# Kernel optimization log

Measured on AMD Instinct MI355X. Metric: run time of the kernel, lower is better.

The kernel has to match this reference:

```python
import jax, jax.numpy as jnp
import numpy as np

N_QUBITS = 12
N_LAYERS = 6
BATCH = 256
INPUT_DIM = 256
OUT_DIM = 64
PI = float(np.pi)


def _ry_mat(a):
    # a: scalar or (B,) real angle -> (...,2,2) complex64 RY matrix
    c, s = jnp.cos(a * 0.5), jnp.sin(a * 0.5)
    return jnp.stack([jnp.stack([c, -s], -1), jnp.stack([s, c], -1)], -2).astype(jnp.complex64)


def _rz_mat(a):
    # diag(e^{-i a/2}, e^{+i a/2})
    em = jnp.exp(-0.5j * a.astype(jnp.complex64))
    ep = jnp.exp(0.5j * a.astype(jnp.complex64))
    z = jnp.zeros_like(em)
    return jnp.stack([jnp.stack([em, z], -1), jnp.stack([z, ep], -1)], -2)


def _apply_1q(state, U, w):
    # shared (2,2) gate on wire w; state: (B, 2, ..., 2)
    s = jnp.moveaxis(state, w + 1, -1)
    s = jnp.einsum('ij,b...j->b...i', U, s)
    return jnp.moveaxis(s, -1, w + 1)


def _apply_1q_batched(state, U, w):
    # per-sample (B,2,2) gate on wire w
    s = jnp.moveaxis(state, w + 1, -1)
    s = jnp.einsum('bij,b...j->b...i', U, s)
    return jnp.moveaxis(s, -1, w + 1)


def _cnot(state, c, t):
    s0 = jnp.take(state, 0, axis=c + 1)
    s1 = jnp.take(state, 1, axis=c + 1)
    t_ax = t + 1 if t < c else t  # target axis index after removing control axis
    s1 = jnp.flip(s1, axis=t_ax)
    return jnp.stack([s0, s1], axis=c + 1)


def _cz(state, c, t):
    idx = [slice(None)] * (N_QUBITS + 1)
    idx[c + 1] = 1
    idx[t + 1] = 1
    return state.at[tuple(idx)].multiply(-1.0)


def _run_circuit(xq, q_weights):
    # xq: (B, n_qubits) in [-1,1]; forward passes xq*pi, circuit multiplies by pi again
    B = xq.shape[0]
    enc = xq * (PI * PI)
    state = jnp.zeros((B, 2 ** N_QUBITS), jnp.complex64).at[:, 0].set(1.0)
    state = state.reshape((B,) + (2,) * N_QUBITS)
    for i in range(N_QUBITS):
        state = _apply_1q_batched(state, _ry_mat(enc[:, i]), i)
    w = q_weights.reshape(N_LAYERS, N_QUBITS, 3)
    for layer in range(N_LAYERS):
        for i in range(N_QUBITS):
            # PennyLane order: RZ(w0) then RY(w1) then RZ(w2) -> U = RZ2 @ RY1 @ RZ0
            U = _rz_mat(w[layer, i, 2]) @ _ry_mat(w[layer, i, 1]) @ _rz_mat(w[layer, i, 0])
            state = _apply_1q(state, U, i)
        for i in range(N_QUBITS):
            state = _cnot(state, i, (i + 1) % N_QUBITS)
        if layer % 2 == 0 and layer < N_LAYERS - 1:
            for i in range(N_QUBITS):
                state = _apply_1q_batched(state, _ry_mat(enc[:, i] * 0.5), i)
        if layer % 2 == 1:
            for i in range(0, N_QUBITS - 2, 2):
                state = _cz(state, i, i + 2)
    # PauliZ expectation on wires 0,1,2
    p = (state.real ** 2 + state.imag ** 2).reshape(B, 2, 2, 2, -1).sum(-1)  # (B,2,2,2)
    z0 = (p[:, 0] - p[:, 1]).sum((-1, -2))
    z1 = (p[:, :, 0] - p[:, :, 1]).sum((-1, -2))
    z2 = (p[:, :, :, 0] - p[:, :, :, 1]).sum((-1, -2))
    return jnp.stack([z0, z1, z2], -1)  # (B, 3) float32


def _layernorm(h, g, b, eps=1e-5):
    mu = h.mean(-1, keepdims=True)
    var = ((h - mu) ** 2).mean(-1, keepdims=True)
    return (h - mu) * jax.lax.rsqrt(var + eps) * g + b


def _forward(x, W1, b1, g_ln, b_ln, W2, b2, W3, b3, q_weights, W4, b4, W5, b5):
    gelu = lambda t: jax.nn.gelu(t, approximate=False)
    h = gelu(x @ W1.T + b1)
    h = _layernorm(h, g_ln, b_ln)
    h = gelu(h @ W2.T + b2)
    xq = jnp.tanh(h @ W3.T + b3)  # (B, n_qubits)
    q = _run_circuit(xq, q_weights)  # (B, 3)
    return gelu(q @ W4.T + b4) @ W5.T + b5  # (B, OUT_DIM)


def setup_inputs() -> dict:
    key = jax.random.key(0)
    ks = jax.random.split(key, 8)
    rn = lambda k, shape, s=0.05: (jax.random.normal(k, shape) * s).astype(jnp.float32)
    return {
        'x': jax.random.normal(ks[0], (BATCH, INPUT_DIM), jnp.float32),
        'W1': rn(ks[1], (128, INPUT_DIM)), 'b1': jnp.zeros(128, jnp.float32),
        'g_ln': jnp.ones(128, jnp.float32), 'b_ln': jnp.zeros(128, jnp.float32),
        'W2': rn(ks[2], (64, 128)), 'b2': jnp.zeros(64, jnp.float32),
        'W3': rn(ks[3], (N_QUBITS, 64)), 'b3': jnp.zeros(N_QUBITS, jnp.float32),
        'q_weights': (jax.random.normal(ks[4], (N_LAYERS * N_QUBITS * 3,)) * 0.1).astype(jnp.float32),
        'W4': rn(ks[5], (32, 3)), 'b4': jnp.zeros(32, jnp.float32),
        'W5': rn(ks[6], (OUT_DIM, 32)), 'b5': jnp.zeros(OUT_DIM, jnp.float32),
    }


def reference(x, W1, b1, g_ln, b_ln, W2, b2, W3, b3, q_weights, W4, b4, W5, b5):
    return _forward(x, W1, b1, g_ln, b_ln, W2, b2, W3, b3, q_weights, W4, b4, W5, b5)
```

## Files before the change

### kernel.cpp

```cpp
#include <hip/hip_runtime.h>
#include <math.h>

#define NQ   12
#define NL   6
#define DIM  4096
#define BATCH 256
#define PI2  9.869604401089358f

__device__ __forceinline__ float geluf(float x) {
    return 0.5f * x * (1.0f + erff(x * 0.70710678118654752f));
}

__device__ __forceinline__ int slotf(int j) { return j + (j >> 4); }

__device__ __forceinline__ float2 cmul(float2 a, float2 b) {
    return make_float2(fmaf(a.x, b.x, -a.y * b.y), fmaf(a.x, b.y, a.y * b.x));
}
__device__ __forceinline__ float2 cadd(float2 a, float2 b) {
    return make_float2(a.x + b.x, a.y + b.y);
}
__device__ __forceinline__ float2 cscale(float2 a, float s) {
    return make_float2(a.x * s, a.y * s);
}

__global__ __launch_bounds__(256)
void qpu_kernel(const float* __restrict__ x,   const float* __restrict__ W1, const float* __restrict__ b1,
                const float* __restrict__ g_ln, const float* __restrict__ b_ln,
                const float* __restrict__ W2,  const float* __restrict__ b2,
                const float* __restrict__ W3,  const float* __restrict__ b3,
                const float* __restrict__ qw,  const float* __restrict__ W4, const float* __restrict__ b4,
                const float* __restrict__ W5,  const float* __restrict__ b5,
                float* __restrict__ out)
{
    __shared__ float2 st[DIM + DIM / 16];
    __shared__ float2 Um[NL * NQ * 4];
    __shared__ float  xs[256];
    __shared__ float  h1n[128];
    __shared__ float  h2s[64];
    __shared__ float  xqs[NQ];
    __shared__ float  musd[2];
    __shared__ float  qv[3];
    __shared__ float  h4s[32];
    __shared__ float  zred[4][3];

    const int t = threadIdx.x;
    const int b = blockIdx.x;

    xs[t] = x[b * 256 + t];
    __syncthreads();

    if (t < 128) {
        const float4* w = (const float4*)(W1 + t * 256);
        float a0 = 0.f, a1 = 0.f, a2 = 0.f, a3 = 0.f;
        #pragma unroll 8
        for (int k = 0; k < 64; k++) {
            float4 wv = w[k];
            const float* xp = &xs[4 * k];
            a0 = fmaf(wv.x, xp[0], a0);
            a1 = fmaf(wv.y, xp[1], a1);
            a2 = fmaf(wv.z, xp[2], a2);
            a3 = fmaf(wv.w, xp[3], a3);
        }
        h1n[t] = geluf((a0 + a1) + (a2 + a3) + b1[t]);
    }
    __syncthreads();

    if (t < 64) {
        float v0 = h1n[t], v1 = h1n[t + 64];
        float s1 = v0 + v1;
        float s2 = fmaf(v0, v0, v1 * v1);
        #pragma unroll
        for (int off = 32; off > 0; off >>= 1) {
            s1 += __shfl_down(s1, off);
            s2 += __shfl_down(s2, off);
        }
        if (t == 0) {
            float mu  = s1 * (1.f / 128.f);
            float var = s2 * (1.f / 128.f) - mu * mu;
            musd[0] = mu;
            musd[1] = rsqrtf(var + 1e-5f);
        }
    }
    __syncthreads();
    if (t < 128) {
        h1n[t] = (h1n[t] - musd[0]) * musd[1] * g_ln[t] + b_ln[t];
    }
    __syncthreads();

    if (t < 64) {
        const float4* w = (const float4*)(W2 + t * 128);
        float a0 = 0.f, a1 = 0.f, a2 = 0.f, a3 = 0.f;
        #pragma unroll 8
        for (int k = 0; k < 32; k++) {
            float4 wv = w[k];
            const float* hp = &h1n[4 * k];
            a0 = fmaf(wv.x, hp[0], a0);
            a1 = fmaf(wv.y, hp[1], a1);
            a2 = fmaf(wv.z, hp[2], a2);
            a3 = fmaf(wv.w, hp[3], a3);
        }
        h2s[t] = geluf((a0 + a1) + (a2 + a3) + b2[t]);
    }
    __syncthreads();

    if (t < NQ) {
        const float4* w = (const float4*)(W3 + t * 64);
        float a0 = 0.f, a1 = 0.f, a2 = 0.f, a3 = 0.f;
        #pragma unroll
        for (int k = 0; k < 16; k++) {
            float4 wv = w[k];
            const float* hp = &h2s[4 * k];
            a0 = fmaf(wv.x, hp[0], a0);
            a1 = fmaf(wv.y, hp[1], a1);
            a2 = fmaf(wv.z, hp[2], a2);
            a3 = fmaf(wv.w, hp[3], a3);
        }
        xqs[t] = tanhf((a0 + a1) + (a2 + a3) + b3[t]);
    }
    __syncthreads();

    if (t < NL * NQ) {
        const int l = t / NQ;
        const int i = t % NQ;
        float a  = qw[t * 3 + 0];
        float bb = qw[t * 3 + 1];
        float c  = qw[t * 3 + 2];
        float sb, cb;   sincosf(0.5f * bb, &sb, &cb);
        float apc = 0.5f * (a + c), amc = 0.5f * (a - c);
        float sapc, capc; sincosf(apc, &sapc, &capc);
        float samc, camc; sincosf(amc, &samc, &camc);
        float2 u00 = make_float2( cb * capc, -cb * sapc);
        float2 u01 = make_float2(-sb * camc, -sb * samc);
        float2 u10 = make_float2( sb * camc, -sb * samc);
        float2 u11 = make_float2( cb * capc,  cb * sapc);

        float theta = 0.f;
        bool merge = false;
        if (l == 0)      { theta = xqs[i] * PI2;        merge = true; }
        else if (l & 1)  { theta = xqs[i] * PI2 * 0.5f; merge = true; }
        if (merge) {
            float sy, cy; sincosf(0.5f * theta, &sy, &cy);
            float2 m00 = cadd(cscale(u00,  cy), cscale(u01, sy));
            float2 m01 = cadd(cscale(u00, -sy), cscale(u01, cy));
            float2 m10 = cadd(cscale(u10,  cy), cscale(u11, sy));
            float2 m11 = cadd(cscale(u10, -sy), cscale(u11, cy));
            u00 = m00; u01 = m01; u10 = m10; u11 = m11;
        }
        Um[t * 4 + 0] = u00;
        Um[t * 4 + 1] = u01;
        Um[t * 4 + 2] = u10;
        Um[t * 4 + 3] = u11;
    }

    #pragma unroll
    for (int m = 0; m < 16; m++) {
        st[slotf(t * 16 + m)] = make_float2(0.f, 0.f);
    }
    if (t == 0) st[slotf(0)] = make_float2(1.f, 0.f);
    __syncthreads();

    for (int l = 0; l < NL; l++) {
        const float2* UL = &Um[l * NQ * 4];

        #pragma unroll
        for (int c = 0; c < 3; c++) {
            const int P    = 8 - 4 * c;
            const int low  = t & ((1 << P) - 1);
            const int base = ((t >> P) << (P + 4)) | low;
            float2 a[16];
            #pragma unroll
            for (int m = 0; m < 16; m++) a[m] = st[slotf(base | (m << P))];
            #pragma unroll
            for (int q = 0; q < 4; q++) {
                const float2 u0 = UL[(4 * c + q) * 4 + 0];
                const float2 u1 = UL[(4 * c + q) * 4 + 1];
                const float2 u2 = UL[(4 * c + q) * 4 + 2];
                const float2 u3 = UL[(4 * c + q) * 4 + 3];
                const int bit = 8 >> q;
                #pragma unroll
                for (int m = 0; m < 16; m++) {
                    if (m & bit) continue;
                    float2 x0 = a[m], x1 = a[m | bit];
                    a[m]       = cadd(cmul(u0, x0), cmul(u1, x1));
                    a[m | bit] = cadd(cmul(u2, x0), cmul(u3, x1));
                }
            }
            #pragma unroll
            for (int m = 0; m < 16; m++) st[slotf(base | (m << P))] = a[m];
            __syncthreads();
        }

        {
            float2 v[16];
            #pragma unroll
            for (int m = 0; m < 16; m++) {
                const int j = t * 16 + m;
                const int src = ((j ^ (j >> 1)) & 0x3FF)
                              | ((((j >> 10) ^ (j >> 11) ^ j) & 1) << 10)
                              | ((((j >> 11) ^ j) & 1) << 11);
                float2 val = st[slotf(src)];
                if (l & 1) {
                    const int cz = j & (j << 2) & 0xAA8;
                    if (__popc(cz) & 1) { val.x = -val.x; val.y = -val.y; }
                }
                v[m] = val;
            }
            __syncthreads();
            #pragma unroll
            for (int m = 0; m < 16; m++) st[slotf(t * 16 + m)] = v[m];
            __syncthreads();
        }
    }

    float s = 0.f;
    #pragma unroll
    for (int m = 0; m < 16; m++) {
        float2 a = st[slotf(t * 16 + m)];
        s = fmaf(a.x, a.x, s);
        s = fmaf(a.y, a.y, s);
    }
    const int j0 = t * 16;
    float z0 = (j0 & (1 << 11)) ? -s : s;
    float z1 = (j0 & (1 << 10)) ? -s : s;
    float z2 = (j0 & (1 <<  9)) ? -s : s;
    #pragma unroll
    for (int off = 32; off > 0; off >>= 1) {
        z0 += __shfl_down(z0, off);
        z1 += __shfl_down(z1, off);
        z2 += __shfl_down(z2, off);
    }
    if ((t & 63) == 0) {
        zred[t >> 6][0] = z0;
        zred[t >> 6][1] = z1;
        zred[t >> 6][2] = z2;
    }
    __syncthreads();
    if (t == 0) {
        qv[0] = zred[0][0] + zred[1][0] + zred[2][0] + zred[3][0];
        qv[1] = zred[0][1] + zred[1][1] + zred[2][1] + zred[3][1];
        qv[2] = zred[0][2] + zred[1][2] + zred[2][2] + zred[3][2];
    }
    __syncthreads();

    if (t < 32) {
        float h = b4[t];
        h = fmaf(qv[0], W4[t * 3 + 0], h);
        h = fmaf(qv[1], W4[t * 3 + 1], h);
        h = fmaf(qv[2], W4[t * 3 + 2], h);
        h4s[t] = geluf(h);
    }
    __syncthreads();
    if (t < 64) {
        float acc = b5[t];
        #pragma unroll
        for (int h = 0; h < 32; h++) acc = fmaf(h4s[h], W5[t * 32 + h], acc);
        out[b * 64 + t] = acc;
    }
}

extern "C" void kernel_launch(void* const* d_in, const int* in_sizes, int n_in,
                              void* d_out, int out_size, void* d_ws, size_t ws_size,
                              hipStream_t stream) {
    (void)in_sizes; (void)n_in; (void)d_ws; (void)ws_size; (void)out_size;
    const float* x    = (const float*)d_in[0];
    const float* W1   = (const float*)d_in[1];
    const float* b1   = (const float*)d_in[2];
    const float* g_ln = (const float*)d_in[3];
    const float* b_ln = (const float*)d_in[4];
    const float* W2   = (const float*)d_in[5];
    const float* b2   = (const float*)d_in[6];
    const float* W3   = (const float*)d_in[7];
    const float* b3   = (const float*)d_in[8];
    const float* qw   = (const float*)d_in[9];
    const float* W4   = (const float*)d_in[10];
    const float* b4   = (const float*)d_in[11];
    const float* W5   = (const float*)d_in[12];
    const float* b5   = (const float*)d_in[13];
    float* out = (float*)d_out;

    qpu_kernel<<<BATCH, 256, 0, stream>>>(x, W1, b1, g_ln, b_ln, W2, b2,
                                          W3, b3, qw, W4, b4, W5, b5, out);
}
```

Before: 112.5 us.

## Use 512 threads with 3-qubit passes, fused permutation loads, ping-pong state buffers

Doubles the block to 512 threads, so each thread holds 8 amplitudes and applies 3 qubit gates per pass over four passes per layer, down from 16 amplitudes and 4 gates over three passes. The CNOT/CZ permutation from the previous layer is folded into the first pass's gather from a second shared state buffer, which removes the separate permute-and-copy step and its two barriers. The Z expectations are computed straight from registers after the last gate pass, skipping the final store. The cost is twice the shared memory for state and one extra barrier-separated pass per layer.

```diff
diff --git a/kernel.cpp b/kernel.cpp
--- a/kernel.cpp
+++ b/kernel.cpp
@@ -5,6 +5,7 @@
 #define NL   6
 #define DIM  4096
 #define BATCH 256
+#define NT   512
 #define PI2  9.869604401089358f
 
 __device__ __forceinline__ float geluf(float x) {
@@ -23,7 +24,7 @@
     return make_float2(a.x * s, a.y * s);
 }
 
-__global__ __launch_bounds__(256)
+__global__ __launch_bounds__(NT)
 void qpu_kernel(const float* __restrict__ x,   const float* __restrict__ W1, const float* __restrict__ b1,
                 const float* __restrict__ g_ln, const float* __restrict__ b_ln,
                 const float* __restrict__ W2,  const float* __restrict__ b2,
@@ -32,7 +33,7 @@
                 const float* __restrict__ W5,  const float* __restrict__ b5,
                 float* __restrict__ out)
 {
-    __shared__ float2 st[DIM + DIM / 16];
+    __shared__ float2 st[2][DIM + DIM / 16];
     __shared__ float2 Um[NL * NQ * 4];
     __shared__ float  xs[256];
     __shared__ float  h1n[128];
@@ -41,12 +42,12 @@
     __shared__ float  musd[2];
     __shared__ float  qv[3];
     __shared__ float  h4s[32];
-    __shared__ float  zred[4][3];
+    __shared__ float  zred[8][3];
 
     const int t = threadIdx.x;
     const int b = blockIdx.x;
 
-    xs[t] = x[b * 256 + t];
+    if (t < 256) xs[t] = x[b * 256 + t];
     __syncthreads();
 
     if (t < 128) {
@@ -151,78 +152,86 @@
         Um[t * 4 + 2] = u10;
         Um[t * 4 + 3] = u11;
     }
-
-    #pragma unroll
-    for (int m = 0; m < 16; m++) {
-        st[slotf(t * 16 + m)] = make_float2(0.f, 0.f);
-    }
-    if (t == 0) st[slotf(0)] = make_float2(1.f, 0.f);
-    __syncthreads();
+    __syncthreads();
+
+    float2 a[8];
+    float z0 = 0.f, z1 = 0.f, z2 = 0.f;
 
     for (int l = 0; l < NL; l++) {
-        const float2* UL = &Um[l * NQ * 4];
-
-        #pragma unroll
-        for (int c = 0; c < 3; c++) {
-            const int P    = 8 - 4 * c;
+        const float2* UL  = &Um[l * NQ * 4];
+        float2*       dst = st[l & 1];
+        const float2* srcb = st[(l & 1) ^ 1];
+
+        #pragma unroll
+        for (int c = 0; c < 4; c++) {
+            const int P    = 9 - 3 * c;
             const int low  = t & ((1 << P) - 1);
-            const int base = ((t >> P) << (P + 4)) | low;
-            float2 a[16];
+            const int base = ((t >> P) << (P + 3)) | low;
+
+            if (c == 0) {
+                if (l == 0) {
+                    #pragma unroll
+                    for (int m = 0; m < 8; m++) a[m] = make_float2(0.f, 0.f);
+                    if (t == 0) a[0] = make_float2(1.f, 0.f);
+                } else {
+                    const bool czl = (l == 2) || (l == 4);
+                    #pragma unroll
+                    for (int m = 0; m < 8; m++) {
+                        const int j = base | (m << 9);
+                        const int src = ((j ^ (j >> 1)) & 0x3FF)
+                                      | ((((j >> 10) ^ (j >> 11) ^ j) & 1) << 10)
+                                      | ((((j >> 11) ^ j) & 1) << 11);
+                        float2 v = srcb[slotf(src)];
+                        if (czl) {
+                            if (__popc(j & (j << 2) & 0xAA8) & 1) { v.x = -v.x; v.y = -v.y; }
+                        }
+                        a[m] = v;
+                    }
+                }
+            } else {
+                #pragma unroll
+                for (int m = 0; m < 8; m++) a[m] = dst[slotf(base | (m << P))];
+            }
+
+            float2 uu[12];
             #pragma unroll
-            for (int m = 0; m < 16; m++) a[m] = st[slotf(base | (m << P))];
+            for (int e = 0; e < 12; e++) uu[e] = UL[(3 * c) * 4 + e];
             #pragma unroll
-            for (int q = 0; q < 4; q++) {
-                const float2 u0 = UL[(4 * c + q) * 4 + 0];
-                const float2 u1 = UL[(4 * c + q) * 4 + 1];
-                const float2 u2 = UL[(4 * c + q) * 4 + 2];
-                const float2 u3 = UL[(4 * c + q) * 4 + 3];
-                const int bit = 8 >> q;
+            for (int k = 0; k < 3; k++) {
+                const float2 u0 = uu[k * 4 + 0];
+                const float2 u1 = uu[k * 4 + 1];
+                const float2 u2 = uu[k * 4 + 2];
+                const float2 u3 = uu[k * 4 + 3];
+                const int bit = 4 >> k;
                 #pragma unroll
-                for (int m = 0; m < 16; m++) {
+                for (int m = 0; m < 8; m++) {
                     if (m & bit) continue;
                     float2 x0 = a[m], x1 = a[m | bit];
                     a[m]       = cadd(cmul(u0, x0), cmul(u1, x1));
                     a[m | bit] = cadd(cmul(u2, x0), cmul(u3, x1));
                 }
             }
-            #pragma unroll
-            for (int m = 0; m < 16; m++) st[slotf(base | (m << P))] = a[m];
-            __syncthreads();
-        }
-
-        {
-            float2 v[16];
-            #pragma unroll
-            for (int m = 0; m < 16; m++) {
-                const int j = t * 16 + m;
-                const int src = ((j ^ (j >> 1)) & 0x3FF)
-                              | ((((j >> 10) ^ (j >> 11) ^ j) & 1) << 10)
-                              | ((((j >> 11) ^ j) & 1) << 11);
-                float2 val = st[slotf(src)];
-                if (l & 1) {
-                    const int cz = j & (j << 2) & 0xAA8;
-                    if (__popc(cz) & 1) { val.x = -val.x; val.y = -val.y; }
-                }
-                v[m] = val;
+
+            if (!(l == NL - 1 && c == 3)) {
+                #pragma unroll
+                for (int m = 0; m < 8; m++) dst[slotf(base | (m << P))] = a[m];
+                __syncthreads();
             }
-            __syncthreads();
-            #pragma unroll
-            for (int m = 0; m < 16; m++) st[slotf(t * 16 + m)] = v[m];
-            __syncthreads();
-        }
-    }
-
-    float s = 0.f;
-    #pragma unroll
-    for (int m = 0; m < 16; m++) {
-        float2 a = st[slotf(t * 16 + m)];
-        s = fmaf(a.x, a.x, s);
-        s = fmaf(a.y, a.y, s);
-    }
-    const int j0 = t * 16;
-    float z0 = (j0 & (1 << 11)) ? -s : s;
-    float z1 = (j0 & (1 << 10)) ? -s : s;
-    float z2 = (j0 & (1 <<  9)) ? -s : s;
+        }
+    }
+
+    {
+        float sp = 0.f, so = 0.f;
+        #pragma unroll
+        for (int m = 0; m < 8; m++) {
+            float p = fmaf(a[m].x, a[m].x, a[m].y * a[m].y);
+            if (__popc(m) & 1) so += p; else sp += p;
+        }
+        const float stot = sp + so;
+        z0 = (__popc(t & 0xFF)  & 1) ? (so - sp) : (sp - so);
+        z1 = (__popc(t & 0x180) & 1) ? -stot : stot;
+        z2 = (__popc(t & 0x1C0) & 1) ? -stot : stot;
+    }
     #pragma unroll
     for (int off = 32; off > 0; off >>= 1) {
         z0 += __shfl_down(z0, off);
@@ -236,9 +245,12 @@
     }
     __syncthreads();
     if (t == 0) {
-        qv[0] = zred[0][0] + zred[1][0] + zred[2][0] + zred[3][0];
-        qv[1] = zred[0][1] + zred[1][1] + zred[2][1] + zred[3][1];
-        qv[2] = zred[0][2] + zred[1][2] + zred[2][2] + zred[3][2];
+        float q0 = 0.f, q1 = 0.f, q2 = 0.f;
+        #pragma unroll
+        for (int w = 0; w < 8; w++) {
+            q0 += zred[w][0]; q1 += zred[w][1]; q2 += zred[w][2];
+        }
+        qv[0] = q0; qv[1] = q1; qv[2] = q2;
     }
     __syncthreads();
 
@@ -278,6 +290,6 @@
     const float* b5   = (const float*)d_in[13];
     float* out = (float*)d_out;
 
-    qpu_kernel<<<BATCH, 256, 0, stream>>>(x, W1, b1, g_ln, b_ln, W2, b2,
-                                          W3, b3, qw, W4, b4, W5, b5, out);
-}
+    qpu_kernel<<<BATCH, NT, 0, stream>>>(x, W1, b1, g_ln, b_ln, W2, b2,
+                                         W3, b3, qw, W4, b4, W5, b5, out);
+}
```

Result: no change. 113.5 us (+0.9%).
